# Kernel tuning notes

Measured on AMD Instinct MI355X. Metric: run time of the kernel, lower is better.

Reference implementation:

```python
import jax, jax.numpy as jnp
import numpy as np

EPS = 1e-5
B, C, T = 128, 64, 1000          # batch, EEG channels, time samples
NCLU, HID, NOUT = 8, 512, 4      # clusters, head hidden dim, outputs (=feature_dim)


def _conv1d(x, w):
    # x: (N, Cin, T), w: (Cout, Cin, K), valid conv along time
    return jax.lax.conv_general_dilated(x, w, (1,), 'VALID',
                                        dimension_numbers=('NCH', 'OIH', 'NCH'))


def _bn(x, g, b, m, v):
    # eval-mode BatchNorm over channel dim of (N, C, T)
    return (x - m[None, :, None]) * (g / jnp.sqrt(v + EPS))[None, :, None] + b[None, :, None]


def _pool3(x):
    # maxpool kernel 3 stride 3 along time
    return jax.lax.reduce_window(x, -jnp.inf, jax.lax.max, (1, 1, 3), (1, 1, 3), 'VALID')


def setup_inputs() -> dict:
    key = jax.random.key(0)
    ks = jax.random.split(key, 12)
    def nrm(k, shape, fan):
        return jax.random.normal(k, shape, jnp.float32) / np.float32(np.sqrt(fan))
    inp = {
        'x': jax.random.normal(ks[0], (B, C, T), jnp.float32),
        'cluster_ids': jax.random.randint(ks[1], (B,), 0, NCLU, jnp.int32),
        # Deep4Net-style backbone params
        'w_time': nrm(ks[2], (25, 1, 10), 10),
        'b_time': jnp.zeros((25,), jnp.float32),
        'w_spat': nrm(ks[3], (25, 25, C), 25 * C),
        'w2': nrm(ks[4], (50, 25, 10), 250),
        'w3': nrm(ks[5], (100, 50, 10), 500),
        'w4': nrm(ks[6], (200, 100, 10), 1000),
        'w_cls': nrm(ks[7], (NOUT, 200, 7), 1400),
        'b_cls': jnp.zeros((NOUT,), jnp.float32),
        # per-cluster expert head params
        'hW1': nrm(ks[8], (NCLU, HID, NOUT), NOUT),
        'hb1': jnp.zeros((NCLU, HID), jnp.float32),
        'hW2': nrm(ks[9], (NCLU, NOUT, HID), HID),
        'hb2': jnp.zeros((NCLU, NOUT), jnp.float32),
        'hg': jnp.ones((NCLU, HID), jnp.float32),
        'hbe': jnp.zeros((NCLU, HID), jnp.float32),
        'hm': jnp.zeros((NCLU, HID), jnp.float32),
        'hv': jnp.ones((NCLU, HID), jnp.float32),
    }
    for i, c in zip((1, 2, 3, 4), (25, 50, 100, 200)):
        inp[f'g{i}'] = jnp.ones((c,), jnp.float32)
        inp[f'be{i}'] = jnp.zeros((c,), jnp.float32)
        inp[f'm{i}'] = jnp.zeros((c,), jnp.float32)
        inp[f'v{i}'] = jnp.ones((c,), jnp.float32)
    return inp


def reference(x, cluster_ids, w_time, b_time, w_spat, w2, w3, w4, w_cls, b_cls,
              hW1, hb1, hW2, hb2, hg, hbe, hm, hv,
              g1, be1, m1, v1, g2, be2, m2, v2, g3, be3, m3, v3, g4, be4, m4, v4):
    b_, c_, t_ = x.shape
    # conv_time: same 25 temporal filters applied per EEG channel -> (B, C, 25, T1)
    h = _conv1d(x.reshape(b_ * c_, 1, t_), w_time) + b_time[None, :, None]
    h = h.reshape(b_, c_, 25, -1)
    # conv_spat: collapse EEG channel axis -> (B, 25, T1)
    z = jnp.einsum('bcft,gfc->bgt', h, w_spat)
    z = _pool3(jax.nn.elu(_bn(z, g1, be1, m1, v1)))
    for w, g, be, m, v in ((w2, g2, be2, m2, v2), (w3, g3, be3, m3, v3), (w4, g4, be4, m4, v4)):
        z = _pool3(jax.nn.elu(_bn(_conv1d(z, w), g, be, m, v)))
    # final_conv_length='auto': classifier conv reduces time dim to 1 -> (B, NOUT)
    feats = (_conv1d(z, w_cls) + b_cls[None, :, None])[:, :, 0]
    # per-sample expert head routing (Linear -> BN(eval) -> ReLU -> [Dropout eval] -> Linear)
    h1 = jnp.einsum('bf,bhf->bh', feats, hW1[cluster_ids]) + hb1[cluster_ids]
    h1 = (h1 - hm[cluster_ids]) * (hg[cluster_ids] / jnp.sqrt(hv[cluster_ids] + EPS)) + hbe[cluster_ids]
    h1 = jax.nn.relu(h1)
    return jnp.einsum('bh,boh->bo', h1, hW2[cluster_ids]) + hb2[cluster_ids]
```

## Files before the change

### kernel.cpp

```cpp
#include <hip/hip_runtime.h>
#include <math.h>

#define EPS_BN 1e-5f

typedef __attribute__((ext_vector_type(8))) short short8;
typedef __attribute__((ext_vector_type(4))) float f32x4;
typedef __attribute__((ext_vector_type(4))) unsigned int uint4v;

__device__ __forceinline__ unsigned short f2bf(float f) {
    unsigned int u = __float_as_uint(f);
    u = (u + 0x7fffu + ((u >> 16) & 1u)) >> 16;
    return (unsigned short)u;
}
__device__ __forceinline__ float bf2f(unsigned short s) {
    return __uint_as_float(((unsigned int)s) << 16);
}
__device__ __forceinline__ float elu1(float y) { return y > 0.f ? y : expm1f(y); }
__device__ __forceinline__ float warp_sum(float v) {
    for (int off = 32; off > 0; off >>= 1) v += __shfl_down(v, off);
    return v;
}

#define UW1 0
#define UW2 20480
#define UW3 40960
#define UW4 122880
#define BB1 0
#define BB2 32
#define BB3 96
#define BB4 224
#define XTG_U 410496
#define Z1G_U 9192320
#define Z2G_U 10544000
#define Z3G_U 11420544
#define Z4G_BYTE 24372992

#define NPREP 1602
#define RS_ZB 36

__global__ __launch_bounds__(256) void kprep_tr(
    const float* __restrict__ x,
    const float* __restrict__ w_time, const float* __restrict__ b_time,
    const float* __restrict__ w_spat,
    const float* __restrict__ w2, const float* __restrict__ w3,
    const float* __restrict__ w4,
    const float* __restrict__ g1, const float* __restrict__ be1,
    const float* __restrict__ m1, const float* __restrict__ v1,
    const float* __restrict__ g2, const float* __restrict__ be2,
    const float* __restrict__ m2, const float* __restrict__ v2,
    const float* __restrict__ g3, const float* __restrict__ be3,
    const float* __restrict__ m3, const float* __restrict__ v3,
    const float* __restrict__ g4, const float* __restrict__ be4,
    const float* __restrict__ m4, const float* __restrict__ v4,
    unsigned short* __restrict__ wsz, float* __restrict__ biasf) {
    __shared__ float tr[64 * 65];
    if (blockIdx.x < NPREP) {
        int idx = blockIdx.x * 256 + threadIdx.x;
        if (idx < 20480) {
            int k = idx >> 11, g = (idx >> 6) & 31, c = idx & 63;
            float val = 0.f;
            if (g < 25) {
                float s = 0.f;
#pragma unroll
                for (int f = 0; f < 25; ++f)
                    s = fmaf(w_spat[g * 1600 + f * 64 + c], w_time[f * 10 + k], s);
                val = s * (g1[g] * rsqrtf(v1[g] + EPS_BN));
            }
            wsz[UW1 + idx] = f2bf(val);
        } else if (idx < 40960) {
            int j = idx - 20480;
            int k = j >> 11, g = (j >> 5) & 63, c = j & 31;
            float val = 0.f;
            if (g < 50 && c < 25)
                val = w2[(g * 25 + c) * 10 + k] * (g2[g] * rsqrtf(v2[g] + EPS_BN));
            wsz[UW2 + j] = f2bf(val);
        } else if (idx < 122880) {
            int j = idx - 40960;
            int k = j >> 13, g = (j >> 6) & 127, c = j & 63;
            float val = 0.f;
            if (g < 100 && c < 50)
                val = w3[(g * 50 + c) * 10 + k] * (g3[g] * rsqrtf(v3[g] + EPS_BN));
            wsz[UW3 + j] = f2bf(val);
        } else if (idx < 409600) {
            int j = idx - 122880;
            int k = j / 28672, r = j % 28672, g = r >> 7, c = r & 127;
            float val = 0.f;
            if (g < 200 && c < 100)
                val = w4[(g * 100 + c) * 10 + k] * (g4[g] * rsqrtf(v4[g] + EPS_BN));
            wsz[UW4 + j] = f2bf(val);
        } else if (idx < 410048) {
            int j = idx - 409600;
            if (j < 32) {
                int g = j; float val = 0.f;
                if (g < 25) {
                    float beff = 0.f;
                    for (int f = 0; f < 25; ++f) {
                        float a = 0.f;
                        for (int c = 0; c < 64; ++c) a += w_spat[g * 1600 + f * 64 + c];
                        beff = fmaf(a, b_time[f], beff);
                    }
                    float sc = g1[g] * rsqrtf(v1[g] + EPS_BN);
                    val = be1[g] - m1[g] * sc + beff * sc;
                }
                biasf[BB1 + g] = val;
            } else if (j < 96) {
                int g = j - 32; float val = 0.f;
                if (g < 50) { float sc = g2[g] * rsqrtf(v2[g] + EPS_BN); val = be2[g] - m2[g] * sc; }
                biasf[BB2 + g] = val;
            } else if (j < 224) {
                int g = j - 96; float val = 0.f;
                if (g < 100) { float sc = g3[g] * rsqrtf(v3[g] + EPS_BN); val = be3[g] - m3[g] * sc; }
                biasf[BB3 + g] = val;
            } else {
                int g = j - 224; float val = 0.f;
                if (g < 200) { float sc = g4[g] * rsqrtf(v4[g] + EPS_BN); val = be4[g] - m4[g] * sc; }
                biasf[BB4 + g] = val;
            }
        }
    } else {
        const int bid = blockIdx.x - NPREP;
        const int b = bid / 17, tile = bid % 17, t = threadIdx.x;
        const int t0 = tile * 64;
        const float* xb = x + b * 64000;
        for (int idx = t; idx < 1024; idx += 256) {
            int c = idx >> 4, q = idx & 15;
            int tg = t0 + 4 * q;
            float4 v = {0.f, 0.f, 0.f, 0.f};
            if (tg + 4 <= 1000) {
                v = *(const float4*)(xb + c * 1000 + tg);
            } else {
                float* pv = (float*)&v;
#pragma unroll
                for (int e = 0; e < 4; ++e)
                    if (tg + e < 1000) pv[e] = xb[c * 1000 + tg + e];
            }
            tr[c * 65 + 4 * q]     = v.x;
            tr[c * 65 + 4 * q + 1] = v.y;
            tr[c * 65 + 4 * q + 2] = v.z;
            tr[c * 65 + 4 * q + 3] = v.w;
        }
        __syncthreads();
        unsigned short* xTg = wsz + XTG_U;
        for (int idx = t; idx < 2048; idx += 256) {
            int tl = idx >> 5, cp = idx & 31;
            int tg = t0 + tl;
            unsigned int pk = 0u;
            if (tg < 1000)
                pk = (unsigned int)f2bf(tr[(2 * cp) * 65 + tl]) |
                     ((unsigned int)f2bf(tr[(2 * cp + 1) * 65 + tl]) << 16);
            if (tg < 1072)
                *(unsigned int*)&xTg[(b * 1072 + tg) * 64 + 2 * cp] = pk;
        }
    }
}

template<int CPAD, int RS, int SP, int TT, int TPC, int NCHUNK, int JMAX,
         int NTCH, int GPAD, int TPOOL, int GSTORE, int NGV, int OUT_RS,
         bool OUT_F32, int NW>
__device__ __forceinline__ void conv_core(
    const unsigned short* xT, const unsigned short* __restrict__ wpk,
    const float* __restrict__ bias,
    unsigned short* zout, float* zoutf, unsigned short* zb,
    int t, int jbeg, int jend, int t0b) {
    const int lane = t & 63;
    const int wv = __builtin_amdgcn_readfirstlane(t >> 6);
    const int lm = lane & 15, h8 = lane >> 4;
    const int gloc = lane & 31, hh = lane >> 5;
    unsigned short* zbw = zb + wv * (48 * RS_ZB);

    for (int job = jbeg + wv; job < jend; job += NW) {
        const int gbi = job / NTCH, tci = job % NTCH;
        const int tl0 = tci * (TT * 16) - t0b;
        const int po0 = tci * (NCHUNK * 16);

        f32x4 acc[TT][2];
#pragma unroll
        for (int i = 0; i < TT; ++i) {
            acc[i][0] = (f32x4){0.f, 0.f, 0.f, 0.f};
            acc[i][1] = (f32x4){0.f, 0.f, 0.f, 0.f};
        }

        const int abase = (tl0 + lm) * RS + h8 * 8;
        const unsigned short* wp = wpk + (gbi * 32 + lm) * CPAD + h8 * 8;
#pragma unroll
        for (int k = 0; k < 10; ++k) {
            short8 w0[SP], w1[SP];
#pragma unroll
            for (int s = 0; s < SP; ++s) {
                w0[s] = *(const short8*)(wp + k * (GPAD * CPAD) + s * 32);
                w1[s] = *(const short8*)(wp + k * (GPAD * CPAD) + 16 * CPAD + s * 32);
            }
#pragma unroll
            for (int s = 0; s < SP; ++s) {
#pragma unroll
                for (int tt = 0; tt < TT; ++tt) {
                    short8 a = *(const short8*)&xT[abase + (tt * 16 + k) * RS + s * 32];
                    acc[tt][0] = __builtin_amdgcn_mfma_f32_16x16x32_bf16(
                        a, w0[s], acc[tt][0], 0, 0, 0);
                    acc[tt][1] = __builtin_amdgcn_mfma_f32_16x16x32_bf16(
                        a, w1[s], acc[tt][1], 0, 0, 0);
                }
            }
        }

        const float bv0 = bias[gbi * 32 + lm];
        const float bv1 = bias[gbi * 32 + 16 + lm];
#pragma unroll
        for (int ch = 0; ch < NCHUNK; ++ch) {
#pragma unroll
            for (int ti = 0; ti < TPC; ++ti) {
                int ttg = ch * TPC + ti;
#pragma unroll
                for (int r = 0; r < 4; ++r) {
                    float v0 = elu1(acc[ttg][0][r] + bv0);
                    float v1 = elu1(acc[ttg][1][r] + bv1);
                    int row = ti * 16 + 4 * h8 + r;
                    zbw[row * RS_ZB + lm] = f2bf(v0);
                    zbw[row * RS_ZB + 16 + lm] = f2bf(v1);
                }
            }
#pragma unroll
            for (int j = 0; j < JMAX; ++j) {
                int po = hh + 2 * j;
                if (3 * po + 2 < TPC * 16) {
                    float q0 = bf2f(zbw[(3 * po) * RS_ZB + gloc]);
                    float q1 = bf2f(zbw[(3 * po + 1) * RS_ZB + gloc]);
                    float q2 = bf2f(zbw[(3 * po + 2) * RS_ZB + gloc]);
                    float mx = fmaxf(q0, fmaxf(q1, q2));
                    int poa = po0 + ch * 16 + po;
                    int ga = gbi * 32 + gloc;
                    if (poa < TPOOL && ga < GSTORE) {
                        if constexpr (OUT_F32)
                            zoutf[poa * OUT_RS + ga] = mx;
                        else
                            zout[poa * OUT_RS + ga] =
                                (ga < NGV) ? f2bf(mx) : (unsigned short)0;
                    }
                }
            }
        }
    }
}

__global__ __launch_bounds__(64) void ks1(
    const unsigned short* __restrict__ wsu, const float* __restrict__ biasf,
    unsigned short* __restrict__ wsz) {
    __shared__ __align__(16) unsigned short xT[112 * 72];
    __shared__ __align__(16) unsigned short zb[48 * RS_ZB];
    const int b = blockIdx.x, tci = blockIdx.y, t = threadIdx.x;
    const int t0b = tci * 96;
    const unsigned short* xTg = wsz + XTG_U + (b * 1072 + t0b) * 64;
    for (int idx = t; idx < 112 * 8; idx += 64) {
        int r = idx >> 3, q = idx & 7;
        *(uint4v*)&xT[r * 72 + 8 * q] = *(const uint4v*)&xTg[r * 64 + 8 * q];
    }
    __syncthreads();
    conv_core<64, 72, 2, 6, 3, 2, 8, 11, 32, 330, 32, 25, 32, false, 1>(
        xT, wsu + UW1, biasf + BB1, wsz + Z1G_U + b * 330 * 32, nullptr, zb,
        t, tci, tci + 1, t0b);
}

__global__ __launch_bounds__(64) void ks2(
    const unsigned short* __restrict__ wsu, const float* __restrict__ biasf,
    unsigned short* __restrict__ wsz) {
    __shared__ __align__(16) unsigned short xT[112 * 40];
    __shared__ __align__(16) unsigned short zb[48 * RS_ZB];
    const int b = blockIdx.x, job = blockIdx.y, t = threadIdx.x;
    const int t0b = (job & 3) * 96;
    const unsigned short* z1g = wsz + Z1G_U + b * 330 * 32;
    for (int idx = t; idx < 112 * 4; idx += 64) {
        int r = idx >> 2, q = idx & 3;
        uint4v v = {0u, 0u, 0u, 0u};
        if (t0b + r < 330) v = *(const uint4v*)&z1g[(t0b + r) * 32 + 8 * q];
        *(uint4v*)&xT[r * 40 + 8 * q] = v;
    }
    __syncthreads();
    conv_core<32, 40, 1, 6, 3, 2, 8, 4, 64, 107, 64, 50, 64, false, 1>(
        xT, wsu + UW2, biasf + BB2, wsz + Z2G_U + b * 107 * 64, nullptr, zb,
        t, job, job + 1, t0b);
}

__global__ __launch_bounds__(64) void ks3(
    const unsigned short* __restrict__ wsu, const float* __restrict__ biasf,
    unsigned short* __restrict__ wsz) {
    __shared__ __align__(16) unsigned short z2t[112 * 72];
    __shared__ __align__(16) unsigned short zb[48 * RS_ZB];
    const int b = blockIdx.x, gbi = blockIdx.y, t = threadIdx.x;
    const unsigned short* z2g = wsz + Z2G_U + b * 107 * 64;
    for (int idx = t; idx < 112 * 8; idx += 64) {
        int r = idx >> 3, q = idx & 7;
        uint4v v = {0u, 0u, 0u, 0u};
        if (r < 107) v = *(const uint4v*)&z2g[r * 64 + 8 * q];
        *(uint4v*)&z2t[r * 72 + 8 * q] = v;
    }
    __syncthreads();
    conv_core<64, 72, 2, 6, 3, 2, 8, 1, 128, 32, 128, 100, 136, false, 1>(
        z2t, wsu + UW3, biasf + BB3, wsz + Z3G_U + b * 44 * 136, nullptr, zb,
        t, gbi, gbi + 1, 0);
}

__global__ __launch_bounds__(64) void ks4(
    const unsigned short* __restrict__ wsu, const float* __restrict__ biasf,
    unsigned short* __restrict__ wsz, float* __restrict__ z4g) {
    __shared__ __align__(16) unsigned short z3t[44 * 136];
    __shared__ __align__(16) unsigned short zb[48 * RS_ZB];
    const int b = blockIdx.x, gbi = blockIdx.y, t = threadIdx.x;
    const unsigned short* z3g = wsz + Z3G_U + b * 44 * 136;
    for (int idx = t; idx < 44 * 17; idx += 64) {
        int r = idx / 17, q = idx % 17;
        uint4v v = {0u, 0u, 0u, 0u};
        if (r < 32) v = *(const uint4v*)&z3g[r * 136 + 8 * q];
        *(uint4v*)&z3t[r * 136 + 8 * q] = v;
    }
    __syncthreads();
    conv_core<128, 136, 4, 2, 2, 1, 4, 1, 224, 7, 200, 200, 200, true, 1>(
        z3t, wsu + UW4, biasf + BB4, nullptr, z4g + b * 1400, zb,
        t, gbi, gbi + 1, 0);
}

__global__ __launch_bounds__(256) void kh(
    const float* __restrict__ z4g,
    const float* __restrict__ w_cls, const float* __restrict__ b_cls,
    const int* __restrict__ cid,
    const float* __restrict__ hW1, const float* __restrict__ hb1,
    const float* __restrict__ hW2, const float* __restrict__ hb2,
    const float* __restrict__ hg, const float* __restrict__ hbe,
    const float* __restrict__ hm, const float* __restrict__ hv,
    float* __restrict__ out) {
    __shared__ float z4f[1400];
    __shared__ float feats[4];
    __shared__ float h1s[512];
    const int b = blockIdx.x, t = threadIdx.x;
    for (int i = t; i < 1400; i += 256) z4f[i] = z4g[b * 1400 + i];
    __syncthreads();

    const int wv = t >> 6, lane = t & 63;
    {
        float p = 0.f;
        for (int i = lane; i < 1400; i += 64) {
            int po = i / 200, g = i - po * 200;
            p = fmaf(z4f[i], w_cls[wv * 1400 + g * 7 + po], p);
        }
        p = warp_sum(p);
        if (lane == 0) feats[wv] = p + b_cls[wv];
    }
    __syncthreads();

    const int c = cid[b];
    const float f0 = feats[0], f1 = feats[1], f2 = feats[2], f3 = feats[3];
    for (int h = t; h < 512; h += 256) {
        const float* w1 = &hW1[(c * 512 + h) * 4];
        float v = f0 * w1[0] + f1 * w1[1] + f2 * w1[2] + f3 * w1[3] + hb1[c * 512 + h];
        float sc = hg[c * 512 + h] * rsqrtf(hv[c * 512 + h] + EPS_BN);
        v = (v - hm[c * 512 + h]) * sc + hbe[c * 512 + h];
        h1s[h] = fmaxf(v, 0.f);
    }
    __syncthreads();
    {
        float p = 0.f;
        for (int i = lane; i < 512; i += 64)
            p = fmaf(h1s[i], hW2[(c * 4 + wv) * 512 + i], p);
        p = warp_sum(p);
        if (lane == 0) out[b * 4 + wv] = p + hb2[c * 4 + wv];
    }
}

extern "C" void kernel_launch(void* const* d_in, const int* in_sizes, int n_in,
                              void* d_out, int out_size, void* d_ws, size_t ws_size,
                              hipStream_t stream) {
    const float* x      = (const float*)d_in[0];
    const int*   cid    = (const int*)d_in[1];
    const float* w_time = (const float*)d_in[2];
    const float* b_time = (const float*)d_in[3];
    const float* w_spat = (const float*)d_in[4];
    const float* w2     = (const float*)d_in[5];
    const float* w3     = (const float*)d_in[6];
    const float* w4     = (const float*)d_in[7];
    const float* w_cls  = (const float*)d_in[8];
    const float* b_cls  = (const float*)d_in[9];
    const float* hW1    = (const float*)d_in[10];
    const float* hb1    = (const float*)d_in[11];
    const float* hW2    = (const float*)d_in[12];
    const float* hb2    = (const float*)d_in[13];
    const float* hg     = (const float*)d_in[14];
    const float* hbe    = (const float*)d_in[15];
    const float* hm     = (const float*)d_in[16];
    const float* hv     = (const float*)d_in[17];
    const float* g1  = (const float*)d_in[18];
    const float* be1 = (const float*)d_in[19];
    const float* m1  = (const float*)d_in[20];
    const float* v1  = (const float*)d_in[21];
    const float* g2  = (const float*)d_in[22];
    const float* be2 = (const float*)d_in[23];
    const float* m2  = (const float*)d_in[24];
    const float* v2  = (const float*)d_in[25];
    const float* g3  = (const float*)d_in[26];
    const float* be3 = (const float*)d_in[27];
    const float* m3  = (const float*)d_in[28];
    const float* v3  = (const float*)d_in[29];
    const float* g4  = (const float*)d_in[30];
    const float* be4 = (const float*)d_in[31];
    const float* m4  = (const float*)d_in[32];
    const float* v4  = (const float*)d_in[33];

    unsigned short* wsz = (unsigned short*)d_ws;
    float* biasf = (float*)((char*)d_ws + 819200);
    float* z4g   = (float*)((char*)d_ws + Z4G_BYTE);
    float* out = (float*)d_out;

    kprep_tr<<<NPREP + 128 * 17, 256, 0, stream>>>(
        x, w_time, b_time, w_spat, w2, w3, w4,
        g1, be1, m1, v1, g2, be2, m2, v2, g3, be3, m3, v3, g4, be4, m4, v4,
        wsz, biasf);

    ks1<<<dim3(128, 11), 64, 0, stream>>>(wsz, biasf, wsz);
    ks2<<<dim3(128, 8), 64, 0, stream>>>(wsz, biasf, wsz);
    ks3<<<dim3(128, 4), 64, 0, stream>>>(wsz, biasf, wsz);
    ks4<<<dim3(128, 7), 64, 0, stream>>>(wsz, biasf, wsz, z4g);
    kh<<<128, 256, 0, stream>>>(z4g, w_cls, b_cls, cid, hW1, hb1, hW2, hb2,
                                hg, hbe, hm, hv, out);
}
```

Baseline: 109.0 us.

## Halve time tiles per block and batch weight loads across five taps

Each conv block now covers 48 time steps instead of 96 (TT 6→3, one pooling chunk), so the grids for layers 1–3 roughly double, giving more blocks and more occupancy. Layer 3 is also split along time instead of one block per batch and group block. In the inner loop, weight fragments for five kernel taps are loaded together before their MFMAs, to hide global load latency. The cost is more halo reloads from overlapping tiles, more redundant weight fetches across blocks, and higher register pressure from the prefetched weights.

```diff
diff --git a/kernel.cpp b/kernel.cpp
--- a/kernel.cpp
+++ b/kernel.cpp
@@ -156,7 +156,7 @@
 
 template<int CPAD, int RS, int SP, int TT, int TPC, int NCHUNK, int JMAX,
          int NTCH, int GPAD, int TPOOL, int GSTORE, int NGV, int OUT_RS,
-         bool OUT_F32, int NW>
+         bool OUT_F32, int NW, int KPRE>
 __device__ __forceinline__ void conv_core(
     const unsigned short* xT, const unsigned short* __restrict__ wpk,
     const float* __restrict__ bias,
@@ -183,22 +183,30 @@
         const int abase = (tl0 + lm) * RS + h8 * 8;
         const unsigned short* wp = wpk + (gbi * 32 + lm) * CPAD + h8 * 8;
 #pragma unroll
-        for (int k = 0; k < 10; ++k) {
-            short8 w0[SP], w1[SP];
-#pragma unroll
-            for (int s = 0; s < SP; ++s) {
-                w0[s] = *(const short8*)(wp + k * (GPAD * CPAD) + s * 32);
-                w1[s] = *(const short8*)(wp + k * (GPAD * CPAD) + 16 * CPAD + s * 32);
-            }
-#pragma unroll
-            for (int s = 0; s < SP; ++s) {
-#pragma unroll
-                for (int tt = 0; tt < TT; ++tt) {
-                    short8 a = *(const short8*)&xT[abase + (tt * 16 + k) * RS + s * 32];
-                    acc[tt][0] = __builtin_amdgcn_mfma_f32_16x16x32_bf16(
-                        a, w0[s], acc[tt][0], 0, 0, 0);
-                    acc[tt][1] = __builtin_amdgcn_mfma_f32_16x16x32_bf16(
-                        a, w1[s], acc[tt][1], 0, 0, 0);
+        for (int ph = 0; ph < 10 / KPRE; ++ph) {
+            short8 w0r[KPRE][SP], w1r[KPRE][SP];
+#pragma unroll
+            for (int kk = 0; kk < KPRE; ++kk) {
+                const int k = ph * KPRE + kk;
+#pragma unroll
+                for (int s = 0; s < SP; ++s) {
+                    w0r[kk][s] = *(const short8*)(wp + k * (GPAD * CPAD) + s * 32);
+                    w1r[kk][s] = *(const short8*)(wp + k * (GPAD * CPAD) + 16 * CPAD + s * 32);
+                }
+            }
+#pragma unroll
+            for (int kk = 0; kk < KPRE; ++kk) {
+                const int k = ph * KPRE + kk;
+#pragma unroll
+                for (int s = 0; s < SP; ++s) {
+#pragma unroll
+                    for (int tt = 0; tt < TT; ++tt) {
+                        short8 a = *(const short8*)&xT[abase + (tt * 16 + k) * RS + s * 32];
+                        acc[tt][0] = __builtin_amdgcn_mfma_f32_16x16x32_bf16(
+                            a, w0r[kk][s], acc[tt][0], 0, 0, 0);
+                        acc[tt][1] = __builtin_amdgcn_mfma_f32_16x16x32_bf16(
+                            a, w1r[kk][s], acc[tt][1], 0, 0, 0);
+                    }
                 }
             }
         }
@@ -245,17 +253,17 @@
 __global__ __launch_bounds__(64) void ks1(
     const unsigned short* __restrict__ wsu, const float* __restrict__ biasf,
     unsigned short* __restrict__ wsz) {
-    __shared__ __align__(16) unsigned short xT[112 * 72];
+    __shared__ __align__(16) unsigned short xT[64 * 72];
     __shared__ __align__(16) unsigned short zb[48 * RS_ZB];
     const int b = blockIdx.x, tci = blockIdx.y, t = threadIdx.x;
-    const int t0b = tci * 96;
+    const int t0b = tci * 48;
     const unsigned short* xTg = wsz + XTG_U + (b * 1072 + t0b) * 64;
-    for (int idx = t; idx < 112 * 8; idx += 64) {
+    for (int idx = t; idx < 64 * 8; idx += 64) {
         int r = idx >> 3, q = idx & 7;
         *(uint4v*)&xT[r * 72 + 8 * q] = *(const uint4v*)&xTg[r * 64 + 8 * q];
     }
     __syncthreads();
-    conv_core<64, 72, 2, 6, 3, 2, 8, 11, 32, 330, 32, 25, 32, false, 1>(
+    conv_core<64, 72, 2, 3, 3, 1, 8, 21, 32, 330, 32, 25, 32, false, 1, 5>(
         xT, wsu + UW1, biasf + BB1, wsz + Z1G_U + b * 330 * 32, nullptr, zb,
         t, tci, tci + 1, t0b);
 }
@@ -263,19 +271,19 @@
 __global__ __launch_bounds__(64) void ks2(
     const unsigned short* __restrict__ wsu, const float* __restrict__ biasf,
     unsigned short* __restrict__ wsz) {
-    __shared__ __align__(16) unsigned short xT[112 * 40];
+    __shared__ __align__(16) unsigned short xT[64 * 40];
     __shared__ __align__(16) unsigned short zb[48 * RS_ZB];
     const int b = blockIdx.x, job = blockIdx.y, t = threadIdx.x;
-    const int t0b = (job & 3) * 96;
+    const int t0b = (job % 7) * 48;
     const unsigned short* z1g = wsz + Z1G_U + b * 330 * 32;
-    for (int idx = t; idx < 112 * 4; idx += 64) {
+    for (int idx = t; idx < 64 * 4; idx += 64) {
         int r = idx >> 2, q = idx & 3;
         uint4v v = {0u, 0u, 0u, 0u};
         if (t0b + r < 330) v = *(const uint4v*)&z1g[(t0b + r) * 32 + 8 * q];
         *(uint4v*)&xT[r * 40 + 8 * q] = v;
     }
     __syncthreads();
-    conv_core<32, 40, 1, 6, 3, 2, 8, 4, 64, 107, 64, 50, 64, false, 1>(
+    conv_core<32, 40, 1, 3, 3, 1, 8, 7, 64, 107, 64, 50, 64, false, 1, 5>(
         xT, wsu + UW2, biasf + BB2, wsz + Z2G_U + b * 107 * 64, nullptr, zb,
         t, job, job + 1, t0b);
 }
@@ -283,20 +291,21 @@
 __global__ __launch_bounds__(64) void ks3(
     const unsigned short* __restrict__ wsu, const float* __restrict__ biasf,
     unsigned short* __restrict__ wsz) {
-    __shared__ __align__(16) unsigned short z2t[112 * 72];
+    __shared__ __align__(16) unsigned short z2t[64 * 72];
     __shared__ __align__(16) unsigned short zb[48 * RS_ZB];
-    const int b = blockIdx.x, gbi = blockIdx.y, t = threadIdx.x;
+    const int b = blockIdx.x, job = blockIdx.y, t = threadIdx.x;
+    const int t0b = (job % 2) * 48;
     const unsigned short* z2g = wsz + Z2G_U + b * 107 * 64;
-    for (int idx = t; idx < 112 * 8; idx += 64) {
+    for (int idx = t; idx < 64 * 8; idx += 64) {
         int r = idx >> 3, q = idx & 7;
         uint4v v = {0u, 0u, 0u, 0u};
-        if (r < 107) v = *(const uint4v*)&z2g[r * 64 + 8 * q];
+        if (t0b + r < 107) v = *(const uint4v*)&z2g[(t0b + r) * 64 + 8 * q];
         *(uint4v*)&z2t[r * 72 + 8 * q] = v;
     }
     __syncthreads();
-    conv_core<64, 72, 2, 6, 3, 2, 8, 1, 128, 32, 128, 100, 136, false, 1>(
+    conv_core<64, 72, 2, 3, 3, 1, 8, 2, 128, 32, 128, 100, 136, false, 1, 5>(
         z2t, wsu + UW3, biasf + BB3, wsz + Z3G_U + b * 44 * 136, nullptr, zb,
-        t, gbi, gbi + 1, 0);
+        t, job, job + 1, t0b);
 }
 
 __global__ __launch_bounds__(64) void ks4(
@@ -313,7 +322,7 @@
         *(uint4v*)&z3t[r * 136 + 8 * q] = v;
     }
     __syncthreads();
-    conv_core<128, 136, 4, 2, 2, 1, 4, 1, 224, 7, 200, 200, 200, true, 1>(
+    conv_core<128, 136, 4, 2, 2, 1, 4, 1, 224, 7, 200, 200, 200, true, 1, 5>(
         z3t, wsu + UW4, biasf + BB4, nullptr, z4g + b * 1400, zb,
         t, gbi, gbi + 1, 0);
 }
@@ -413,9 +422,9 @@
         g1, be1, m1, v1, g2, be2, m2, v2, g3, be3, m3, v3, g4, be4, m4, v4,
         wsz, biasf);
 
-    ks1<<<dim3(128, 11), 64, 0, stream>>>(wsz, biasf, wsz);
-    ks2<<<dim3(128, 8), 64, 0, stream>>>(wsz, biasf, wsz);
-    ks3<<<dim3(128, 4), 64, 0, stream>>>(wsz, biasf, wsz);
+    ks1<<<dim3(128, 21), 64, 0, stream>>>(wsz, biasf, wsz);
+    ks2<<<dim3(128, 14), 64, 0, stream>>>(wsz, biasf, wsz);
+    ks3<<<dim3(128, 8), 64, 0, stream>>>(wsz, biasf, wsz);
     ks4<<<dim3(128, 7), 64, 0, stream>>>(wsz, biasf, wsz, z4g);
     kh<<<128, 256, 0, stream>>>(z4g, w_cls, b_cls, cid, hW1, hb1, hW2, hb2,
                                 hg, hbe, hm, hv, out);
```

Measured after the change: 102.4 us. -6.0%, faster.
